# Performance work log

Measured on AMD Instinct MI355X. Metric: run time of the kernel, lower is better.

## Reference

```python
import jax, jax.numpy as jnp
import numpy as np
from jax import lax

IN_CH, OUT_CH, K, STYLE_DIM = 512, 512, 3, 512
B, H, W = 16, 64, 64
SCALE = 1.0 / np.sqrt(IN_CH * K * K).astype(np.float32)
EPS = 1e-8


def setup_inputs() -> dict:
    key = jax.random.key(0)
    k1, k2, k3, k4 = jax.random.split(key, 4)
    return {
        "x": jax.random.normal(k1, (B, IN_CH, H, W), dtype=jnp.float32),
        "style": jax.random.normal(k2, (B, STYLE_DIM), dtype=jnp.float32),
        "weight": jax.random.normal(k3, (1, OUT_CH, IN_CH, K, K), dtype=jnp.float32),
        "mod_w": jax.random.normal(k4, (IN_CH, STYLE_DIM), dtype=jnp.float32) / np.sqrt(STYLE_DIM),
        "mod_b": jnp.ones((IN_CH,), dtype=jnp.float32),
    }


def reference(x, style, weight, mod_w, mod_b):
    b, cin, h, w = x.shape
    out_ch = weight.shape[1]
    k = weight.shape[-1]
    pad = k // 2
    # style projection: (B, in_channel)
    s = style @ mod_w.T + mod_b
    # modulated weight: (B, out, in, k, k)
    wmod = SCALE * weight * s[:, None, :, None, None]
    # demodulation: rsqrt of sum of squares over (in, kh, kw)
    demod = lax.rsqrt(jnp.sum(wmod * wmod, axis=(2, 3, 4)) + EPS)
    wmod = wmod * demod[:, :, None, None, None]
    # grouped conv with groups = batch
    wflat = wmod.reshape(b * out_ch, cin, k, k)
    xin = x.reshape(1, b * cin, h, w)
    out = lax.conv_general_dilated(
        xin, wflat,
        window_strides=(1, 1),
        padding=[(pad, pad), (pad, pad)],
        dimension_numbers=("NCHW", "OIHW", "NCHW"),
        feature_group_count=b,
    )
    return out.reshape(b, out_ch, h, w)
```

## Files before the change

kernel.cpp:

```cpp
#include <hip/hip_runtime.h>
#include <hip/hip_bf16.h>
#include <cstdint>
#include <cstddef>

typedef __bf16 bf16x8 __attribute__((ext_vector_type(8)));
typedef float f32x4 __attribute__((ext_vector_type(4)));
typedef float f32x16 __attribute__((ext_vector_type(16)));

#define MOD_SCALE 1.4731391e-02f
#define EPSF 1e-8f

__global__ __launch_bounds__(512) void k_style(
    const float* __restrict__ style, const float* __restrict__ mod_w,
    const float* __restrict__ mod_b, float* __restrict__ s)
{
  __shared__ float st[512];
  const int b = blockIdx.x, i = threadIdx.x;
  st[i] = style[b*512 + i];
  __syncthreads();
  const float4* mw = (const float4*)(mod_w + (size_t)i*512);
  float acc = 0.f;
  #pragma unroll 8
  for (int j = 0; j < 128; ++j) {
    float4 v = mw[j];
    acc += v.x*st[4*j] + v.y*st[4*j+1] + v.z*st[4*j+2] + v.w*st[4*j+3];
  }
  s[b*512 + i] = acc + mod_b[i];
}

__global__ __launch_bounds__(256) void k_weight(
    const float* __restrict__ weight, float* __restrict__ w2,
    __hip_bfloat16* __restrict__ Wb)
{
  const int o = blockIdx.x, t = threadIdx.x;
  #pragma unroll
  for (int h = 0; h < 2; ++h) {
    const int i = t + h*256;
    const float* wp = weight + ((size_t)o*512 + i)*9;
    float sq = 0.f;
    #pragma unroll
    for (int kk = 0; kk < 9; ++kk) {
      float v = wp[kk];
      sq += v*v;
      Wb[((size_t)kk*512 + o)*512 + i] = __float2bfloat16(v * MOD_SCALE);
    }
    w2[(size_t)o*512 + i] = sq;
  }
}

__global__ __launch_bounds__(256) void k_demod(
    const float* __restrict__ s, const float* __restrict__ w2,
    float* __restrict__ demod)
{
  __shared__ float s2[512];
  const int b = blockIdx.x, t = threadIdx.x;
  {
    float a = s[b*512 + t];        s2[t]     = a*a;
    float c = s[b*512 + t + 256];  s2[t+256] = c*c;
  }
  __syncthreads();
  #pragma unroll
  for (int h = 0; h < 2; ++h) {
    const int o = t + h*256;
    const float4* wp = (const float4*)(w2 + (size_t)o*512);
    float acc = 0.f;
    #pragma unroll 8
    for (int j = 0; j < 128; ++j) {
      float4 v = wp[j];
      acc += v.x*s2[4*j] + v.y*s2[4*j+1] + v.z*s2[4*j+2] + v.w*s2[4*j+3];
    }
    demod[b*512 + o] = rsqrtf(MOD_SCALE*MOD_SCALE*acc + EPSF);
  }
}

__global__ __launch_bounds__(256) void k_xm(
    const float* __restrict__ x, const float* __restrict__ s,
    __hip_bfloat16* __restrict__ Xm)
{
  __shared__ __hip_bfloat16 T[64][40];
  const int bid = blockIdx.x;
  const int cb = bid & 15, y = (bid >> 4) & 63, b = bid >> 10;
  const int ic0 = cb*32;
  const int t = threadIdx.x;
  const int i = t >> 3, x0 = (t & 7)*8;
  const float sv = s[b*512 + ic0 + i];
  const float4* xp = (const float4*)(x + (size_t)(b*512 + ic0 + i)*4096 + y*64 + x0);
  float4 v0 = xp[0], v1 = xp[1];
  float vals[8] = {v0.x, v0.y, v0.z, v0.w, v1.x, v1.y, v1.z, v1.w};
  #pragma unroll
  for (int j = 0; j < 8; ++j) T[x0+j][i] = __float2bfloat16(vals[j]*sv);

  const float4 z4 = make_float4(0.f, 0.f, 0.f, 0.f);
  if (t < 8) {
    const int side = t >> 2, j = t & 3;
    float4* hz = (float4*)(Xm + (((size_t)(b*66 + (y+1))*66 + side*65)*512 + ic0 + j*8));
    *hz = z4;
  }
  if (y == 0) {
    for (int idx = t; idx < 264; idx += 256) {
      const int px = idx >> 2, j = idx & 3;
      float4* hz = (float4*)(Xm + (((size_t)(b*66 + 0)*66 + px)*512 + ic0 + j*8));
      *hz = z4;
    }
  }
  if (y == 63) {
    for (int idx = t; idx < 264; idx += 256) {
      const int px = idx >> 2, j = idx & 3;
      float4* hz = (float4*)(Xm + (((size_t)(b*66 + 65)*66 + px)*512 + ic0 + j*8));
      *hz = z4;
    }
  }

  __syncthreads();
  const int p = t >> 2, c = (t & 3)*8;
  __hip_bfloat16* dst = Xm + (((size_t)(b*66 + (y+1))*66 + (p+1))*512 + ic0 + c);
  *(float4*)dst = *(const float4*)&T[p][c];
}

#define VMC(n) asm volatile("s_waitcnt vmcnt(" #n ")" ::: "memory")

__global__ __launch_bounds__(512, 2) void k_conv(
    const __hip_bfloat16* __restrict__ Wb,
    const __hip_bfloat16* __restrict__ Xm,
    const float* __restrict__ demod,
    float* __restrict__ out)
{
  __shared__ __hip_bfloat16 lds[2][2][16384];

  const int orig = blockIdx.x;
  const int swz = (orig & 7)*64 + (orig >> 3);
  const int b  = swz >> 5;
  const int nt = (swz & 31) >> 1;
  const int mt = swz & 1;
  const int o0 = mt*256, y0 = nt*4;

  const int tid = threadIdx.x;
  const int l = tid & 63;
  const int w = tid >> 6;
  const int wm = w >> 2;
  const int wn = w & 3;

  const int srow = tid >> 3;
  const int tq   = (tid & 7) ^ (srow & 7);
  const char* WbC = (const char*)Wb;
  const char* XmC = (const char*)Xm;

  const int rowb = ((l >> 5) << 4) | (l & 15);
  const int lb4  = (l >> 4) & 1;
  const int sB   = (l & 7) << 4;

  #define STAGE_A(tau, h, bfi) do { \
    const int kk_ = (tau) >> 3; \
    const int cb_ = ((tau) & 7) << 7; \
    _Pragma("unroll") \
    for (int it_ = 0; it_ < 2; ++it_) { \
      const int R_ = it_*64 + srow; \
      const int gr_ = (R_ & 0x6F) | ((tq & 1) << 4); \
      const int gc_ = ((tq & 6) | ((R_ >> 4) & 1)) << 4; \
      const char* src_ = WbC + (size_t)(kk_*512 + o0 + (h)*128 + gr_)*1024 + cb_ + gc_; \
      __builtin_amdgcn_global_load_lds( \
        (__attribute__((address_space(1))) void*)src_, \
        (__attribute__((address_space(3))) void*)((char*)&lds[bfi][0][0] + (h)*16384 + it_*8192 + w*1024), \
        16, 0, 0); \
    } \
  } while(0)

  #define STAGE_B(tau, h, bfi) do { \
    const int kk_ = (tau) >> 3; \
    const int cb_ = ((tau) & 7) << 7; \
    const int dy_ = kk_/3 - 1, dx_ = kk_ - (kk_/3)*3 - 1; \
    _Pragma("unroll") \
    for (int it_ = 0; it_ < 2; ++it_) { \
      const int R_ = it_*64 + srow; \
      const int gr_ = (R_ & 0x6F) | ((tq & 1) << 4); \
      const int gc_ = ((tq & 6) | ((R_ >> 4) & 1)) << 4; \
      const int py_ = y0 + (h)*2 + (gr_ >> 6) + dy_ + 1; \
      const int px_ = (gr_ & 63) + dx_ + 1; \
      const char* src_ = XmC + ((size_t)((b*66 + py_)*66 + px_))*1024 + cb_ + gc_; \
      __builtin_amdgcn_global_load_lds( \
        (__attribute__((address_space(1))) void*)src_, \
        (__attribute__((address_space(3))) void*)((char*)&lds[bfi][1][0] + (h)*16384 + it_*8192 + w*1024), \
        16, 0, 0); \
    } \
  } while(0)

  #define STAGE_TILE(tau, bfi) do { \
    STAGE_A(tau, 0, bfi); STAGE_A(tau, 1, bfi); \
    STAGE_B(tau, 0, bfi); STAGE_B(tau, 1, bfi); \
  } while(0)

  f32x16 acc[4][2] = {};

  #define TILE(BFI, STG, VMCW, BAR) do { \
    const char* Ab_ = (const char*)&lds[BFI][0][0]; \
    const char* Bb_ = (const char*)&lds[BFI][1][0]; \
    STG; \
    _Pragma("unroll") \
    for (int p_ = 0; p_ < 4; ++p_) { \
      bf16x8 a_[4], b_[2]; \
      const int kc_ = (((p_ << 1) | lb4) << 4) ^ sB; \
      _Pragma("unroll") \
      for (int j_ = 0; j_ < 4; ++j_) \
        a_[j_] = *(const bf16x8*)(Ab_ + (j_ >> 1)*16384 + wm*8192 + (j_ & 1)*4096 \
                                  + rowb*128 + kc_); \
      _Pragma("unroll") \
      for (int nh_ = 0; nh_ < 2; ++nh_) \
        b_[nh_] = *(const bf16x8*)(Bb_ + nh_*16384 + wn*4096 + rowb*128 + kc_); \
      __builtin_amdgcn_s_setprio(1); \
      _Pragma("unroll") \
      for (int j_ = 0; j_ < 4; ++j_) \
        _Pragma("unroll") \
        for (int nh_ = 0; nh_ < 2; ++nh_) \
          acc[j_][nh_] = __builtin_amdgcn_mfma_f32_32x32x16_bf16( \
              a_[j_], b_[nh_], acc[j_][nh_], 0, 0, 0); \
      __builtin_amdgcn_s_setprio(0); \
    } \
    VMCW; \
    if (BAR) __builtin_amdgcn_s_barrier(); \
  } while(0)

  STAGE_TILE(0, 0);
  VMC(0);
  __builtin_amdgcn_s_barrier();

  #pragma unroll 1
  for (int tt = 0; tt < 35; ++tt) {
    const int t = tt*2;
    TILE(0, STAGE_TILE(t+1, 1), VMC(0), 1);
    TILE(1, STAGE_TILE(t+2, 0), VMC(0), 1);
  }
  TILE(0, STAGE_TILE(71, 1), VMC(0), 1);
  TILE(1, (void)0, (void)0, 0);

  const int lr = l & 31;
  #pragma unroll
  for (int am = 0; am < 4; ++am) {
    const int om = o0 + (am >> 1)*128 + wm*64 + (am & 1)*32 + ((l >> 5) << 2);
    #pragma unroll
    for (int NH = 0; NH < 2; ++NH) {
      const int nc = NH*128 + wn*32 + lr;
      const int y = y0 + (nc >> 6), xx = nc & 63;
      #pragma unroll
      for (int g = 0; g < 4; ++g) {
        const f32x4 dm = *(const f32x4*)(demod + b*512 + om + 8*g);
        float* op = out + (size_t)(b*512 + om + 8*g)*4096 + y*64 + xx;
        #pragma unroll
        for (int j = 0; j < 4; ++j)
          op[(size_t)j*4096] = acc[am][NH][g*4 + j] * dm[j];
      }
    }
  }
  #undef TILE
  #undef STAGE_TILE
  #undef STAGE_A
  #undef STAGE_B
}

extern "C" void kernel_launch(void* const* d_in, const int* in_sizes, int n_in,
                              void* d_out, int out_size, void* d_ws, size_t ws_size,
                              hipStream_t stream)
{
  const float* x      = (const float*)d_in[0];
  const float* style  = (const float*)d_in[1];
  const float* weight = (const float*)d_in[2];
  const float* mod_w  = (const float*)d_in[3];
  const float* mod_b  = (const float*)d_in[4];
  float* out = (float*)d_out;

  char* ws = (char*)d_ws;
  float* s            = (float*)(ws);
  float* demod        = (float*)(ws + 32768);
  float* w2           = (float*)(ws + 65536);
  __hip_bfloat16* Wb  = (__hip_bfloat16*)(ws + 1114112);
  __hip_bfloat16* Xm  = (__hip_bfloat16*)(ws + 5832704);

  k_style <<<16,    512, 0, stream>>>(style, mod_w, mod_b, s);
  k_weight<<<512,   256, 0, stream>>>(weight, w2, Wb);
  k_demod <<<16,    256, 0, stream>>>(s, w2, demod);
  k_xm    <<<16384, 256, 0, stream>>>(x, s, Xm);
  k_conv  <<<512,   512, 0, stream>>>(Wb, Xm, demod, out);
}
```

Baseline: 391.8 us.

## Load weight fragments directly to registers in MFMA layout, bypassing LDS

```diff
diff --git a/kernel.cpp b/kernel.cpp
--- a/kernel.cpp
+++ b/kernel.cpp
@@ -30,19 +30,24 @@
 
 __global__ __launch_bounds__(256) void k_weight(
     const float* __restrict__ weight, float* __restrict__ w2,
-    __hip_bfloat16* __restrict__ Wb)
+    __hip_bfloat16* __restrict__ WF)
 {
   const int o = blockIdx.x, t = threadIdx.x;
   #pragma unroll
   for (int h = 0; h < 2; ++h) {
     const int i = t + h*256;
     const float* wp = weight + ((size_t)o*512 + i)*9;
+    const int g = o >> 5;
+    const int lane = (o & 31) | (((i >> 3) & 1) << 5);
+    const int e = i & 7;
+    const int cc = i >> 6, ks = (i >> 4) & 3;
+    __hip_bfloat16* dst = WF + ((((size_t)(cc*4 + ks))*16 + g)*64 + lane)*8 + e;
     float sq = 0.f;
     #pragma unroll
     for (int kk = 0; kk < 9; ++kk) {
       float v = wp[kk];
       sq += v*v;
-      Wb[((size_t)kk*512 + o)*512 + i] = __float2bfloat16(v * MOD_SCALE);
+      dst[(size_t)kk*262144] = __float2bfloat16(v * MOD_SCALE);
     }
     w2[(size_t)o*512 + i] = sq;
   }
@@ -118,14 +123,15 @@
 }
 
 #define VMC(n) asm volatile("s_waitcnt vmcnt(" #n ")" ::: "memory")
+#define FENCE() asm volatile("" ::: "memory")
 
 __global__ __launch_bounds__(512, 2) void k_conv(
-    const __hip_bfloat16* __restrict__ Wb,
+    const __hip_bfloat16* __restrict__ WF,
     const __hip_bfloat16* __restrict__ Xm,
     const float* __restrict__ demod,
     float* __restrict__ out)
 {
-  __shared__ __hip_bfloat16 lds[2][2][16384];
+  __shared__ __hip_bfloat16 lds[2][16384];
 
   const int orig = blockIdx.x;
   const int swz = (orig & 7)*64 + (orig >> 3);
@@ -142,28 +148,13 @@
 
   const int srow = tid >> 3;
   const int tq   = (tid & 7) ^ (srow & 7);
-  const char* WbC = (const char*)Wb;
   const char* XmC = (const char*)Xm;
+
+  const char* WFC = (const char*)WF + (size_t)(mt*8 + wm*4)*1024 + l*16;
 
   const int rowb = ((l >> 5) << 4) | (l & 15);
   const int lb4  = (l >> 4) & 1;
   const int sB   = (l & 7) << 4;
-
-  #define STAGE_A(tau, h, bfi) do { \
-    const int kk_ = (tau) >> 3; \
-    const int cb_ = ((tau) & 7) << 7; \
-    _Pragma("unroll") \
-    for (int it_ = 0; it_ < 2; ++it_) { \
-      const int R_ = it_*64 + srow; \
-      const int gr_ = (R_ & 0x6F) | ((tq & 1) << 4); \
-      const int gc_ = ((tq & 6) | ((R_ >> 4) & 1)) << 4; \
-      const char* src_ = WbC + (size_t)(kk_*512 + o0 + (h)*128 + gr_)*1024 + cb_ + gc_; \
-      __builtin_amdgcn_global_load_lds( \
-        (__attribute__((address_space(1))) void*)src_, \
-        (__attribute__((address_space(3))) void*)((char*)&lds[bfi][0][0] + (h)*16384 + it_*8192 + w*1024), \
-        16, 0, 0); \
-    } \
-  } while(0)
 
   #define STAGE_B(tau, h, bfi) do { \
     const int kk_ = (tau) >> 3; \
@@ -179,63 +170,88 @@
       const char* src_ = XmC + ((size_t)((b*66 + py_)*66 + px_))*1024 + cb_ + gc_; \
       __builtin_amdgcn_global_load_lds( \
         (__attribute__((address_space(1))) void*)src_, \
-        (__attribute__((address_space(3))) void*)((char*)&lds[bfi][1][0] + (h)*16384 + it_*8192 + w*1024), \
+        (__attribute__((address_space(3))) void*)((char*)&lds[bfi][0] + (h)*16384 + it_*8192 + w*1024), \
         16, 0, 0); \
     } \
   } while(0)
 
-  #define STAGE_TILE(tau, bfi) do { \
-    STAGE_A(tau, 0, bfi); STAGE_A(tau, 1, bfi); \
+  #define STAGE_TILE_B(tau, bfi) do { \
     STAGE_B(tau, 0, bfi); STAGE_B(tau, 1, bfi); \
   } while(0)
 
-  f32x16 acc[4][2] = {};
-
-  #define TILE(BFI, STG, VMCW, BAR) do { \
-    const char* Ab_ = (const char*)&lds[BFI][0][0]; \
-    const char* Bb_ = (const char*)&lds[BFI][1][0]; \
-    STG; \
-    _Pragma("unroll") \
-    for (int p_ = 0; p_ < 4; ++p_) { \
-      bf16x8 a_[4], b_[2]; \
-      const int kc_ = (((p_ << 1) | lb4) << 4) ^ sB; \
+  #define ISSA(t, hh, dst) do { \
+    _Pragma("unroll") \
+    for (int k2_ = 0; k2_ < 2; ++k2_) { \
+      const char* pA_ = WFC + (size_t)((t)*4 + (hh)*2 + k2_)*16384; \
       _Pragma("unroll") \
-      for (int j_ = 0; j_ < 4; ++j_) \
-        a_[j_] = *(const bf16x8*)(Ab_ + (j_ >> 1)*16384 + wm*8192 + (j_ & 1)*4096 \
-                                  + rowb*128 + kc_); \
+      for (int am_ = 0; am_ < 4; ++am_) \
+        dst[k2_][am_] = *(const bf16x8*)(pA_ + am_*1024); \
+    } \
+  } while(0)
+
+  #define RDB(Bb, hh, dst) do { \
+    _Pragma("unroll") \
+    for (int k2_ = 0; k2_ < 2; ++k2_) { \
+      const int kc_ = ((((hh)*2 + k2_) << 1 | lb4) << 4) ^ sB; \
       _Pragma("unroll") \
       for (int nh_ = 0; nh_ < 2; ++nh_) \
-        b_[nh_] = *(const bf16x8*)(Bb_ + nh_*16384 + wn*4096 + rowb*128 + kc_); \
-      __builtin_amdgcn_s_setprio(1); \
+        dst[k2_][nh_] = *(const bf16x8*)((Bb) + nh_*16384 + wn*4096 + rowb*128 + kc_); \
+    } \
+  } while(0)
+
+  #define MM(k2, av, bv) do { \
+    _Pragma("unroll") \
+    for (int am_ = 0; am_ < 4; ++am_) \
       _Pragma("unroll") \
-      for (int j_ = 0; j_ < 4; ++j_) \
-        _Pragma("unroll") \
-        for (int nh_ = 0; nh_ < 2; ++nh_) \
-          acc[j_][nh_] = __builtin_amdgcn_mfma_f32_32x32x16_bf16( \
-              a_[j_], b_[nh_], acc[j_][nh_], 0, 0, 0); \
-      __builtin_amdgcn_s_setprio(0); \
-    } \
-    VMCW; \
-    if (BAR) __builtin_amdgcn_s_barrier(); \
-  } while(0)
-
-  STAGE_TILE(0, 0);
-  VMC(0);
+      for (int nh_ = 0; nh_ < 2; ++nh_) \
+        acc[am_][nh_] = __builtin_amdgcn_mfma_f32_32x32x16_bf16( \
+            av[k2][am_], bv[k2][nh_], acc[am_][nh_], 0, 0, 0); \
+  } while(0)
+
+  f32x16 acc[4][2] = {};
+  bf16x8 aH0[2][4], aH1[2][4], b_[2][2];
+
+  STAGE_TILE_B(0, 0);
+  FENCE();
+  ISSA(0, 0, aH0);
+  VMC(8);
   __builtin_amdgcn_s_barrier();
 
   #pragma unroll 1
-  for (int tt = 0; tt < 35; ++tt) {
-    const int t = tt*2;
-    TILE(0, STAGE_TILE(t+1, 1), VMC(0), 1);
-    TILE(1, STAGE_TILE(t+2, 0), VMC(0), 1);
-  }
-  TILE(0, STAGE_TILE(71, 1), VMC(0), 1);
-  TILE(1, (void)0, (void)0, 0);
+  for (int t = 0; t < 71; ++t) {
+    const char* Bb_ = (const char*)&lds[t & 1][0];
+    RDB(Bb_, 0, b_);
+    ISSA(t, 1, aH1);
+    VMC(8);
+    MM(0, aH0, b_);
+    MM(1, aH0, b_);
+    RDB(Bb_, 1, b_);
+    STAGE_TILE_B(t+1, (t & 1)^1);
+    FENCE();
+    ISSA(t+1, 0, aH0);
+    VMC(12);
+    MM(0, aH1, b_);
+    MM(1, aH1, b_);
+    VMC(8);
+    __builtin_amdgcn_s_barrier();
+  }
+  {
+    const char* Bb_ = (const char*)&lds[1][0];
+    RDB(Bb_, 0, b_);
+    ISSA(71, 1, aH1);
+    VMC(8);
+    MM(0, aH0, b_);
+    MM(1, aH0, b_);
+    RDB(Bb_, 1, b_);
+    VMC(0);
+    MM(0, aH1, b_);
+    MM(1, aH1, b_);
+  }
 
   const int lr = l & 31;
   #pragma unroll
   for (int am = 0; am < 4; ++am) {
-    const int om = o0 + (am >> 1)*128 + wm*64 + (am & 1)*32 + ((l >> 5) << 2);
+    const int om = o0 + wm*128 + am*32 + ((l >> 5) << 2);
     #pragma unroll
     for (int NH = 0; NH < 2; ++NH) {
       const int nc = NH*128 + wn*32 + lr;
@@ -250,9 +266,10 @@
       }
     }
   }
-  #undef TILE
-  #undef STAGE_TILE
-  #undef STAGE_A
+  #undef MM
+  #undef RDB
+  #undef ISSA
+  #undef STAGE_TILE_B
   #undef STAGE_B
 }
 
@@ -271,12 +288,12 @@
   float* s            = (float*)(ws);
   float* demod        = (float*)(ws + 32768);
   float* w2           = (float*)(ws + 65536);
-  __hip_bfloat16* Wb  = (__hip_bfloat16*)(ws + 1114112);
+  __hip_bfloat16* WF  = (__hip_bfloat16*)(ws + 1114112);
   __hip_bfloat16* Xm  = (__hip_bfloat16*)(ws + 5832704);
 
   k_style <<<16,    512, 0, stream>>>(style, mod_w, mod_b, s);
-  k_weight<<<512,   256, 0, stream>>>(weight, w2, Wb);
+  k_weight<<<512,   256, 0, stream>>>(weight, w2, WF);
   k_demod <<<16,    256, 0, stream>>>(s, w2, demod);
   k_xm    <<<16384, 256, 0, stream>>>(x, s, Xm);
-  k_conv  <<<512,   512, 0, stream>>>(Wb, Xm, demod, out);
-}
+  k_conv  <<<512,   512, 0, stream>>>(WF, Xm, demod, out);
+}
```

Measured after the change: 412.4 us. 5.2% more time.
